# Kernel optimization log

Measured on AMD Instinct MI355X. Metric: run time of the kernel, lower is better.

## Reference

```python
import jax, jax.numpy as jnp
import numpy as np

N_NODES = 10000


def gcn_conv(x, W, b, src, dst, n):
    # GCNConv (PyG defaults): linear transform, add self-loops, symmetric norm,
    # scatter-add aggregation at target nodes, then bias.
    h = x @ W  # [n, out]
    # degree with self-loops: 1 (self) + count of incoming edges per target node
    deg = jnp.ones((n,), h.dtype).at[dst].add(1.0)
    dinv = jax.lax.rsqrt(deg)  # deg >= 1 always
    norm = dinv[src] * dinv[dst]  # [E]
    # edge messages + self-loop contribution (norm_ii = dinv_i^2)
    agg = jnp.zeros_like(h).at[dst].add(h[src] * norm[:, None])
    agg = agg + h * (dinv * dinv)[:, None]
    return agg + b


def setup_inputs() -> dict:
    key = jax.random.key(0)
    ks = jax.random.split(key, 8)
    d_in, d_hid, d_out = 512, 512, 100
    n, e = N_NODES, 160000
    x = jax.random.normal(ks[0], (n, d_in), dtype=jnp.float32)
    edge_index = jax.random.randint(ks[1], (2, e), 0, n, dtype=jnp.int64)
    s1 = 1.0 / np.sqrt(d_in)
    s2 = 1.0 / np.sqrt(d_hid)
    W1 = jax.random.uniform(ks[2], (d_in, d_hid), jnp.float32, -s1, s1)
    b1 = jnp.zeros((d_hid,), jnp.float32)
    W2 = jax.random.uniform(ks[3], (d_hid, d_hid), jnp.float32, -s2, s2)
    b2 = jnp.zeros((d_hid,), jnp.float32)
    Wc = jax.random.uniform(ks[4], (d_hid, d_out), jnp.float32, -s2, s2)
    bc = jax.random.uniform(ks[5], (d_out,), jnp.float32, -s2, s2)
    return {"x": x, "edge_index": edge_index, "W1": W1, "b1": b1,
            "W2": W2, "b2": b2, "Wc": Wc, "bc": bc}


def reference(x, edge_index, W1, b1, W2, b2, Wc, bc):
    src, dst = edge_index[0], edge_index[1]
    n = x.shape[0]
    h = gcn_conv(x, W1, b1, src, dst, n)
    h = jax.nn.relu(h)  # dropout is identity in eval mode
    h = gcn_conv(h, W2, b2, src, dst, n)
    return h @ Wc + bc
```

## Files before the change

kernel.cpp:

```cpp
#include <hip/hip_runtime.h>
#include <hip/hip_bf16.h>
#include <stdint.h>

typedef __bf16 bf16_t;
typedef bf16_t bf16x8 __attribute__((ext_vector_type(8)));
typedef float f32x4 __attribute__((ext_vector_type(4)));

#define NN 10000
#define ELLCAP 64

__device__ __forceinline__ float b2f(unsigned short u) {
  union { unsigned int i; float f; } c; c.i = ((unsigned int)u) << 16; return c.f;
}
__device__ __forceinline__ unsigned short f2b(float f) {
  union { float f; unsigned int i; } c; c.f = f;
  unsigned int x = c.i;
  x += 0x7FFFu + ((x >> 16) & 1u);
  return (unsigned short)(x >> 16);
}
__device__ __forceinline__ uint4 cvt8(float4 a, float4 b) {
  uint4 r;
  r.x = (unsigned int)f2b(a.x) | ((unsigned int)f2b(a.y) << 16);
  r.y = (unsigned int)f2b(a.z) | ((unsigned int)f2b(a.w) << 16);
  r.z = (unsigned int)f2b(b.x) | ((unsigned int)f2b(b.y) << 16);
  r.w = (unsigned int)f2b(b.z) | ((unsigned int)f2b(b.w) << 16);
  return r;
}
__device__ __forceinline__ void load_lds16(const void* g, void* l) {
  __builtin_amdgcn_global_load_lds(
      (const __attribute__((address_space(1))) unsigned int*)g,
      (__attribute__((address_space(3))) unsigned int*)l, 16, 0, 0);
}
__device__ __forceinline__ f32x4 mfma16(bf16x8 a, bf16x8 b, f32x4 c) {
  return __builtin_amdgcn_mfma_f32_16x16x32_bf16(a, b, c, 0, 0, 0);
}

template <bool SCALED>
__device__ void gemm64(const unsigned short* __restrict__ A, const unsigned short* __restrict__ Bt,
                       unsigned short* __restrict__ C, const int* __restrict__ cntp,
                       int M, int Ncols, int ldc, int tm, int tn,
                       unsigned short* __restrict__ As, unsigned short* __restrict__ Bs)
{
  const int tid = threadIdx.x;
  const int lane = tid & 63;
  const int wn = tid >> 6;
  const int quad = lane >> 4, l15 = lane & 15;

  const int r0 = tid >> 2, kc = tid & 3;
  int ga = tm * 64 + r0;  if (ga > M - 1) ga = M - 1;
  const int gb0 = tn * 128 + r0;
  const int gb1 = tn * 128 + 64 + r0;
  const unsigned short* gA  = A + (size_t)ga * 512 + kc * 8;
  const unsigned short* gB0 = Bt + (size_t)gb0 * 512 + kc * 8;
  const unsigned short* gB1 = Bt + (size_t)gb1 * 512 + kc * 8;
  const int loff  = r0 * 32 + kc * 8;
  const int loff1 = (64 + r0) * 32 + kc * 8;
  const int ABUF = 64 * 32, BBUF = 128 * 32;

  f32x4 acc[4][2];
  #pragma unroll
  for (int i = 0; i < 4; i++)
    #pragma unroll
    for (int j = 0; j < 2; j++) {
      f32x4 z = {0.f, 0.f, 0.f, 0.f};
      acc[i][j] = z;
    }

  load_lds16(gA,  &As[loff]);
  load_lds16(gB0, &Bs[loff]);
  load_lds16(gB1, &Bs[loff1]);
  __syncthreads();

  for (int it = 0; it < 16; ++it) {
    const int ca = (it & 1) * ABUF, cb = (it & 1) * BBUF;
    if (it < 15) {
      const int k1 = (it + 1) * 32;
      const int na = ((it & 1) ^ 1) * ABUF, nb = ((it & 1) ^ 1) * BBUF;
      load_lds16(gA + k1,  &As[na + loff]);
      load_lds16(gB0 + k1, &Bs[nb + loff]);
      load_lds16(gB1 + k1, &Bs[nb + loff1]);
    }
    bf16x8 af[4], bfr[2];
    #pragma unroll
    for (int i = 0; i < 4; i++)
      af[i] = *(const bf16x8*)&As[ca + (i * 16 + l15) * 32 + quad * 8];
    #pragma unroll
    for (int j = 0; j < 2; j++)
      bfr[j] = *(const bf16x8*)&Bs[cb + (wn * 32 + j * 16 + l15) * 32 + quad * 8];
    #pragma unroll
    for (int i = 0; i < 4; i++)
      #pragma unroll
      for (int j = 0; j < 2; j++)
        acc[i][j] = mfma16(af[i], bfr[j], acc[i][j]);
    __syncthreads();
  }

  #pragma unroll
  for (int i = 0; i < 4; i++) {
    #pragma unroll
    for (int r = 0; r < 4; r++) {
      const int row = tm * 64 + i * 16 + quad * 4 + r;
      if (row < M) {
        float dv = 1.f;
        if (SCALED) {
          int c = cntp[row]; if (c > ELLCAP) c = ELLCAP;
          dv = rsqrtf((float)(1 + c));
        }
        #pragma unroll
        for (int j = 0; j < 2; j++) {
          const int col = tn * 128 + wn * 32 + j * 16 + l15;
          if (col < Ncols)
            C[(size_t)row * ldc + col] = f2b(acc[i][j][r] * dv);
        }
      }
    }
  }
}

__device__ void wtrans_tile(const float* __restrict__ W, unsigned short* __restrict__ Wt,
                            int ncols, int tr0, int tc0)
{
  __shared__ float tile[64][65];
  const int t = threadIdx.x;
  const int r = t >> 2, c4 = t & 3;
  #pragma unroll
  for (int i = 0; i < 4; i++) {
    int col = c4 * 16 + i * 4;
    int gc = tc0 + col;
    float4 v;
    if (gc + 3 < ncols) {
      v = *(const float4*)&W[(size_t)(tr0 + r) * ncols + gc];
    } else {
      v.x = (gc + 0 < ncols) ? W[(size_t)(tr0 + r) * ncols + gc + 0] : 0.f;
      v.y = (gc + 1 < ncols) ? W[(size_t)(tr0 + r) * ncols + gc + 1] : 0.f;
      v.z = (gc + 2 < ncols) ? W[(size_t)(tr0 + r) * ncols + gc + 2] : 0.f;
      v.w = (gc + 3 < ncols) ? W[(size_t)(tr0 + r) * ncols + gc + 3] : 0.f;
    }
    tile[r][col] = v.x; tile[r][col + 1] = v.y;
    tile[r][col + 2] = v.z; tile[r][col + 3] = v.w;
  }
  __syncthreads();
  const int o = t >> 2;
  #pragma unroll
  for (int i = 0; i < 4; i++) {
    int k = c4 * 16 + i * 4;
    ushort4 u;
    u.x = f2b(tile[k + 0][o]); u.y = f2b(tile[k + 1][o]);
    u.z = f2b(tile[k + 2][o]); u.w = f2b(tile[k + 3][o]);
    *(ushort4*)&Wt[(size_t)(tc0 + o) * 512 + tr0 + k] = u;
  }
}

__global__ __launch_bounds__(256)
void prep_fill(const float* __restrict__ W1, const float* __restrict__ Wc,
               const float* __restrict__ W2, const float* __restrict__ x,
               const int* __restrict__ src, const int* __restrict__ dst,
               int* __restrict__ cnt, int* __restrict__ ell,
               unsigned short* __restrict__ W1t, unsigned short* __restrict__ Wct,
               unsigned short* __restrict__ w2b, unsigned short* __restrict__ xb, int E)
{
  if (blockIdx.x < 64) { wtrans_tile(W1, W1t, 512, (blockIdx.x >> 3) * 64, (blockIdx.x & 7) * 64); return; }
  if (blockIdx.x < 80) { int b = blockIdx.x - 64; wtrans_tile(Wc, Wct, 100, (b >> 1) * 64, (b & 1) * 64); return; }
  const int t0 = (blockIdx.x - 80) * 256 + threadIdx.x;
  const int FT = 256 * 256;
  const float4* W24 = (const float4*)W2;
  uint4* w2b4 = (uint4*)w2b;
  for (int i = t0; i < 512 * 512 / 8; i += FT)
    w2b4[i] = cvt8(W24[i * 2], W24[i * 2 + 1]);
  const float4* x4 = (const float4*)x;
  uint4* xb4 = (uint4*)xb;
  for (int i = t0; i < NN * 512 / 8; i += FT)
    xb4[i] = cvt8(x4[i * 2], x4[i * 2 + 1]);
  for (int e = t0; e < E; e += FT) {
    int s = src[e], d = dst[e];
    int pos = atomicAdd(&cnt[d], 1);
    if (pos < ELLCAP) ell[d * ELLCAP + pos] = s;
  }
}

__global__ __launch_bounds__(256)
void gemm1_fold(const unsigned short* __restrict__ xb, const unsigned short* __restrict__ W1t,
                unsigned short* __restrict__ B2, const int* __restrict__ cnt,
                const unsigned short* __restrict__ Wct, const unsigned short* __restrict__ w2b,
                unsigned short* __restrict__ W2WcT,
                const float* __restrict__ b2, const float* __restrict__ Wc,
                const float* __restrict__ bc, float* __restrict__ bias2c)
{
  __shared__ __align__(16) unsigned short As[2 * 64 * 32];
  __shared__ __align__(16) unsigned short Bs[2 * 128 * 32];
  const int b = blockIdx.x;
  if (b < 628) {
    gemm64<true>(xb, W1t, B2, cnt, NN, 512, 512, b >> 2, b & 3, As, Bs);
  } else if (b < 636) {
    const int g = b - 628;
    gemm64<false>(Wct, w2b, W2WcT, nullptr, 128, 512, 512, g >> 2, g & 3, As, Bs);
  } else {
    const int j = threadIdx.x;
    if (j < 128) {
      float s = 0.f;
      if (j < 100) {
        s = bc[j];
        for (int k = 0; k < 512; k++) s = fmaf(b2[k], Wc[k * 100 + j], s);
      }
      bias2c[j] = s;
    }
  }
}

__device__ __forceinline__ void add8(float* a, uint4 v) {
  a[0] += b2f((unsigned short)(v.x & 0xffffu));
  a[1] += b2f((unsigned short)(v.x >> 16));
  a[2] += b2f((unsigned short)(v.y & 0xffffu));
  a[3] += b2f((unsigned short)(v.y >> 16));
  a[4] += b2f((unsigned short)(v.z & 0xffffu));
  a[5] += b2f((unsigned short)(v.z >> 16));
  a[6] += b2f((unsigned short)(v.w & 0xffffu));
  a[7] += b2f((unsigned short)(v.w >> 16));
}

__global__ __launch_bounds__(256)
void gather1(const unsigned short* __restrict__ h, const int* __restrict__ cnt,
             const int* __restrict__ ell, const float* __restrict__ bias,
             unsigned short* __restrict__ outb, int n)
{
  int node = blockIdx.x * 4 + (threadIdx.x >> 6);
  if (node >= n) return;
  const int lane = threadIdx.x & 63;
  const int c8 = lane * 8;

  int cd = cnt[node]; if (cd > ELLCAP) cd = ELLCAP;
  const float dinv = rsqrtf((float)(1 + cd));
  uint4 hv = *(const uint4*)&h[(size_t)node * 512 + c8];
  float a[8] = {0.f, 0.f, 0.f, 0.f, 0.f, 0.f, 0.f, 0.f};
  add8(a, hv);

  const int* row = ell + node * ELLCAP;
  int j = 0;
  for (; j + 8 <= cd; j += 8) {
    int ss[8]; uint4 vv[8];
    #pragma unroll
    for (int q = 0; q < 8; q++) ss[q] = row[j + q];
    #pragma unroll
    for (int q = 0; q < 8; q++) vv[q] = *(const uint4*)&h[(size_t)ss[q] * 512 + c8];
    #pragma unroll
    for (int q = 0; q < 8; q++) add8(a, vv[q]);
  }
  for (; j < cd; ++j) {
    int s = row[j];
    uint4 v = *(const uint4*)&h[(size_t)s * 512 + c8];
    add8(a, v);
  }

  const float4* bp = (const float4*)&bias[c8];
  float4 b0 = bp[0], b1 = bp[1];
  float bb[8] = {b0.x, b0.y, b0.z, b0.w, b1.x, b1.y, b1.z, b1.w};
  #pragma unroll
  for (int q = 0; q < 8; q++) a[q] = fmaxf(fmaf(a[q], dinv, bb[q]), 0.f);
  uint4 o;
  o.x = (unsigned int)f2b(a[0]) | ((unsigned int)f2b(a[1]) << 16);
  o.y = (unsigned int)f2b(a[2]) | ((unsigned int)f2b(a[3]) << 16);
  o.z = (unsigned int)f2b(a[4]) | ((unsigned int)f2b(a[5]) << 16);
  o.w = (unsigned int)f2b(a[6]) | ((unsigned int)f2b(a[7]) << 16);
  *(uint4*)&outb[(size_t)node * 512 + c8] = o;
}

__global__ __launch_bounds__(256)
void gemm2c(const unsigned short* __restrict__ B1, const unsigned short* __restrict__ W2WcT,
            unsigned short* __restrict__ Z, const int* __restrict__ cnt)
{
  __shared__ __align__(16) unsigned short As[2 * 64 * 32];
  __shared__ __align__(16) unsigned short Bs[2 * 128 * 32];
  gemm64<true>(B1, W2WcT, Z, cnt, NN, 128, 128, blockIdx.x, 0, As, Bs);
}

__global__ __launch_bounds__(256)
void gather2c(const unsigned short* __restrict__ Z, const int* __restrict__ cnt,
              const int* __restrict__ ell, const float* __restrict__ bias2c,
              float* __restrict__ out, int n)
{
  int node = blockIdx.x * 4 + (threadIdx.x >> 6);
  if (node >= n) return;
  const int lane = threadIdx.x & 63;
  const int c2 = lane * 2;

  int cd = cnt[node]; if (cd > ELLCAP) cd = ELLCAP;
  const float dinv = rsqrtf((float)(1 + cd));
  unsigned int hv = *(const unsigned int*)&Z[(size_t)node * 128 + c2];
  float a0 = b2f((unsigned short)(hv & 0xffffu));
  float a1 = b2f((unsigned short)(hv >> 16));

  const int* row = ell + node * ELLCAP;
  int j = 0;
  for (; j + 8 <= cd; j += 8) {
    int ss[8]; unsigned int vv[8];
    #pragma unroll
    for (int q = 0; q < 8; q++) ss[q] = row[j + q];
    #pragma unroll
    for (int q = 0; q < 8; q++) vv[q] = *(const unsigned int*)&Z[(size_t)ss[q] * 128 + c2];
    #pragma unroll
    for (int q = 0; q < 8; q++) {
      a0 += b2f((unsigned short)(vv[q] & 0xffffu));
      a1 += b2f((unsigned short)(vv[q] >> 16));
    }
  }
  for (; j < cd; ++j) {
    int s = row[j];
    unsigned int v = *(const unsigned int*)&Z[(size_t)s * 128 + c2];
    a0 += b2f((unsigned short)(v & 0xffffu));
    a1 += b2f((unsigned short)(v >> 16));
  }
  if (c2 < 100) {
    const float2 bb = *(const float2*)&bias2c[c2];
    *(float2*)&out[(size_t)node * 100 + c2] =
        make_float2(fmaf(a0, dinv, bb.x), fmaf(a1, dinv, bb.y));
  }
}

extern "C" void kernel_launch(void* const* d_in, const int* in_sizes, int n_in,
                              void* d_out, int out_size, void* d_ws, size_t ws_size,
                              hipStream_t stream) {
  const float* x  = (const float*)d_in[0];
  const int*   ei = (const int*)d_in[1];
  const float* W1 = (const float*)d_in[2];
  const float* b1 = (const float*)d_in[3];
  const float* W2 = (const float*)d_in[4];
  const float* b2 = (const float*)d_in[5];
  const float* Wc = (const float*)d_in[6];
  const float* bc = (const float*)d_in[7];
  float* out = (float*)d_out;

  const int n = NN;
  const int E = in_sizes[1] / 2;
  const int* src = ei;
  const int* dst = ei + E;

  char* w = (char*)d_ws;
  int* cnt = (int*)w;                       w += ((n * 4 + 255) / 256) * 256;
  int* ell = (int*)w;                       w += ((n * ELLCAP * 4 + 255) / 256) * 256;
  float* bias2c = (float*)w;                w += 512;
  unsigned short* W1t = (unsigned short*)w; w += 512 * 512 * 2;
  unsigned short* Wct = (unsigned short*)w; w += 128 * 512 * 2;
  unsigned short* w2b = (unsigned short*)w; w += 512 * 512 * 2;
  unsigned short* W2WcT = (unsigned short*)w; w += 128 * 512 * 2;
  unsigned short* B1  = (unsigned short*)w; w += (size_t)n * 512 * 2;
  unsigned short* B2  = (unsigned short*)w; w += (size_t)n * 512 * 2;
  unsigned short* Z   = (unsigned short*)w; w += (size_t)n * 128 * 2;

  unsigned short* xb = B1;

  const int nb_g = (n + 3) / 4;

  hipMemsetAsync(cnt, 0, n * sizeof(int), stream);
  prep_fill<<<336, 256, 0, stream>>>(W1, Wc, W2, x, src, dst, cnt, ell, W1t, Wct, w2b, xb, E);
  gemm1_fold<<<637, 256, 0, stream>>>(xb, W1t, B2, cnt, Wct, w2b, W2WcT, b2, Wc, bc, bias2c);
  gather1<<<nb_g, 256, 0, stream>>>(B2, cnt, ell, b1, B1, n);
  gemm2c<<<157, 256, 0, stream>>>(B1, W2WcT, Z, cnt);
  gather2c<<<nb_g, 256, 0, stream>>>(Z, cnt, ell, bias2c, out, n);
}
```

Measured before the change: 159.1 us.

## Fuse all stages into one persistent kernel with grid barriers

Replaces the five separate kernel launches with a single persistent kernel of 512 blocks. The stages are separated by atomic-counter grid barriers, and each stage loops over its tiles or node blocks. This removes launch overhead and inter-kernel gaps. In exchange, the grid-wide barriers cost something, the spin-wait depends on all 512 blocks being co-resident (with launch_bounds occupancy 2), and fewer blocks run the large GEMM1 phase (637 tiles over 512 blocks).

```diff
diff --git a/kernel.cpp b/kernel.cpp
--- a/kernel.cpp
+++ b/kernel.cpp
@@ -8,6 +8,8 @@
 
 #define NN 10000
 #define ELLCAP 64
+#define GRID 512
+#define NBV 2500
 
 __device__ __forceinline__ float b2f(unsigned short u) {
   union { unsigned int i; float f; } c; c.i = ((unsigned int)u) << 16; return c.f;
@@ -33,6 +35,17 @@
 }
 __device__ __forceinline__ f32x4 mfma16(bf16x8 a, bf16x8 b, f32x4 c) {
   return __builtin_amdgcn_mfma_f32_16x16x32_bf16(a, b, c, 0, 0, 0);
+}
+
+__device__ __forceinline__ void gridbar(int* __restrict__ bar, int idx) {
+  __syncthreads();
+  if (threadIdx.x == 0) {
+    __threadfence();
+    __hip_atomic_fetch_add(&bar[idx], 1, __ATOMIC_ACQ_REL, __HIP_MEMORY_SCOPE_AGENT);
+    while (__hip_atomic_load(&bar[idx], __ATOMIC_ACQUIRE, __HIP_MEMORY_SCOPE_AGENT) < GRID)
+      __builtin_amdgcn_s_sleep(1);
+  }
+  __syncthreads();
 }
 
 template <bool SCALED>
@@ -118,9 +131,8 @@
 }
 
 __device__ void wtrans_tile(const float* __restrict__ W, unsigned short* __restrict__ Wt,
-                            int ncols, int tr0, int tc0)
-{
-  __shared__ float tile[64][65];
+                            int ncols, int tr0, int tc0, float (*tile)[65])
+{
   const int t = threadIdx.x;
   const int r = t >> 2, c4 = t & 3;
   #pragma unroll
@@ -149,20 +161,17 @@
     u.z = f2b(tile[k + 2][o]); u.w = f2b(tile[k + 3][o]);
     *(ushort4*)&Wt[(size_t)(tc0 + o) * 512 + tr0 + k] = u;
   }
-}
-
-__global__ __launch_bounds__(256)
-void prep_fill(const float* __restrict__ W1, const float* __restrict__ Wc,
-               const float* __restrict__ W2, const float* __restrict__ x,
-               const int* __restrict__ src, const int* __restrict__ dst,
-               int* __restrict__ cnt, int* __restrict__ ell,
-               unsigned short* __restrict__ W1t, unsigned short* __restrict__ Wct,
-               unsigned short* __restrict__ w2b, unsigned short* __restrict__ xb, int E)
-{
-  if (blockIdx.x < 64) { wtrans_tile(W1, W1t, 512, (blockIdx.x >> 3) * 64, (blockIdx.x & 7) * 64); return; }
-  if (blockIdx.x < 80) { int b = blockIdx.x - 64; wtrans_tile(Wc, Wct, 100, (b >> 1) * 64, (b & 1) * 64); return; }
-  const int t0 = (blockIdx.x - 80) * 256 + threadIdx.x;
-  const int FT = 256 * 256;
+  __syncthreads();
+}
+
+__device__ void prep_stream(int b, int nstream, const float* __restrict__ W2,
+                            const float* __restrict__ x, const int* __restrict__ src,
+                            const int* __restrict__ dst, int* __restrict__ cnt,
+                            int* __restrict__ ell, unsigned short* __restrict__ w2b,
+                            unsigned short* __restrict__ xb, int E)
+{
+  const int t0 = b * 256 + threadIdx.x;
+  const int FT = nstream * 256;
   const float4* W24 = (const float4*)W2;
   uint4* w2b4 = (uint4*)w2b;
   for (int i = t0; i < 512 * 512 / 8; i += FT)
@@ -178,32 +187,17 @@
   }
 }
 
-__global__ __launch_bounds__(256)
-void gemm1_fold(const unsigned short* __restrict__ xb, const unsigned short* __restrict__ W1t,
-                unsigned short* __restrict__ B2, const int* __restrict__ cnt,
-                const unsigned short* __restrict__ Wct, const unsigned short* __restrict__ w2b,
-                unsigned short* __restrict__ W2WcT,
-                const float* __restrict__ b2, const float* __restrict__ Wc,
-                const float* __restrict__ bc, float* __restrict__ bias2c)
-{
-  __shared__ __align__(16) unsigned short As[2 * 64 * 32];
-  __shared__ __align__(16) unsigned short Bs[2 * 128 * 32];
-  const int b = blockIdx.x;
-  if (b < 628) {
-    gemm64<true>(xb, W1t, B2, cnt, NN, 512, 512, b >> 2, b & 3, As, Bs);
-  } else if (b < 636) {
-    const int g = b - 628;
-    gemm64<false>(Wct, w2b, W2WcT, nullptr, 128, 512, 512, g >> 2, g & 3, As, Bs);
-  } else {
-    const int j = threadIdx.x;
-    if (j < 128) {
-      float s = 0.f;
-      if (j < 100) {
-        s = bc[j];
-        for (int k = 0; k < 512; k++) s = fmaf(b2[k], Wc[k * 100 + j], s);
-      }
-      bias2c[j] = s;
-    }
+__device__ void bias_fold(const float* __restrict__ b2, const float* __restrict__ Wc,
+                          const float* __restrict__ bc, float* __restrict__ bias2c)
+{
+  const int j = threadIdx.x;
+  if (j < 128) {
+    float s = 0.f;
+    if (j < 100) {
+      s = bc[j];
+      for (int k = 0; k < 512; k++) s = fmaf(b2[k], Wc[k * 100 + j], s);
+    }
+    bias2c[j] = s;
   }
 }
 
@@ -218,13 +212,12 @@
   a[7] += b2f((unsigned short)(v.w >> 16));
 }
 
-__global__ __launch_bounds__(256)
-void gather1(const unsigned short* __restrict__ h, const int* __restrict__ cnt,
-             const int* __restrict__ ell, const float* __restrict__ bias,
-             unsigned short* __restrict__ outb, int n)
-{
-  int node = blockIdx.x * 4 + (threadIdx.x >> 6);
-  if (node >= n) return;
+__device__ void gather1_body(int vb, const unsigned short* __restrict__ h,
+                             const int* __restrict__ cnt, const int* __restrict__ ell,
+                             const float* __restrict__ bias, unsigned short* __restrict__ outb)
+{
+  int node = vb * 4 + (threadIdx.x >> 6);
+  if (node >= NN) return;
   const int lane = threadIdx.x & 63;
   const int c8 = lane * 8;
 
@@ -264,22 +257,12 @@
   *(uint4*)&outb[(size_t)node * 512 + c8] = o;
 }
 
-__global__ __launch_bounds__(256)
-void gemm2c(const unsigned short* __restrict__ B1, const unsigned short* __restrict__ W2WcT,
-            unsigned short* __restrict__ Z, const int* __restrict__ cnt)
-{
-  __shared__ __align__(16) unsigned short As[2 * 64 * 32];
-  __shared__ __align__(16) unsigned short Bs[2 * 128 * 32];
-  gemm64<true>(B1, W2WcT, Z, cnt, NN, 128, 128, blockIdx.x, 0, As, Bs);
-}
-
-__global__ __launch_bounds__(256)
-void gather2c(const unsigned short* __restrict__ Z, const int* __restrict__ cnt,
-              const int* __restrict__ ell, const float* __restrict__ bias2c,
-              float* __restrict__ out, int n)
-{
-  int node = blockIdx.x * 4 + (threadIdx.x >> 6);
-  if (node >= n) return;
+__device__ void gather2c_body(int vb, const unsigned short* __restrict__ Z,
+                              const int* __restrict__ cnt, const int* __restrict__ ell,
+                              const float* __restrict__ bias2c, float* __restrict__ out)
+{
+  int node = vb * 4 + (threadIdx.x >> 6);
+  if (node >= NN) return;
   const int lane = threadIdx.x & 63;
   const int c2 = lane * 2;
 
@@ -314,6 +297,44 @@
     *(float2*)&out[(size_t)node * 100 + c2] =
         make_float2(fmaf(a0, dinv, bb.x), fmaf(a1, dinv, bb.y));
   }
+}
+
+__global__ __launch_bounds__(256, 2)
+void fused(const float* __restrict__ x, const int* __restrict__ src, const int* __restrict__ dst,
+           const float* __restrict__ W1, const float* __restrict__ b1,
+           const float* __restrict__ W2, const float* __restrict__ b2,
+           const float* __restrict__ Wc, const float* __restrict__ bc,
+           float* __restrict__ out, int* __restrict__ bar, int* __restrict__ cnt,
+           int* __restrict__ ell, float* __restrict__ bias2c,
+           unsigned short* __restrict__ W1t, unsigned short* __restrict__ Wct,
+           unsigned short* __restrict__ w2b, unsigned short* __restrict__ W2WcT,
+           unsigned short* __restrict__ B1, unsigned short* __restrict__ B2,
+           unsigned short* __restrict__ Z, unsigned short* __restrict__ xb, int E)
+{
+  __shared__ __align__(16) unsigned char smem[24576];
+  unsigned short* As = (unsigned short*)smem;
+  unsigned short* Bs = (unsigned short*)(smem + 8192);
+  const int b = blockIdx.x;
+
+  if (b < 64)      wtrans_tile(W1, W1t, 512, (b >> 3) * 64, (b & 7) * 64, (float(*)[65])smem);
+  else if (b < 80) { int t = b - 64; wtrans_tile(Wc, Wct, 100, (t >> 1) * 64, (t & 1) * 64, (float(*)[65])smem); }
+  else             prep_stream(b - 80, GRID - 80, W2, x, src, dst, cnt, ell, w2b, xb, E);
+  gridbar(bar, 0);
+
+  for (int t = b; t < 637; t += GRID) {
+    if (t < 628)      gemm64<true>(xb, W1t, B2, cnt, NN, 512, 512, t >> 2, t & 3, As, Bs);
+    else if (t < 636) { int g = t - 628; gemm64<false>(Wct, w2b, W2WcT, nullptr, 128, 512, 512, g >> 2, g & 3, As, Bs); }
+    else              bias_fold(b2, Wc, bc, bias2c);
+  }
+  gridbar(bar, 1);
+
+  for (int vb = b; vb < NBV; vb += GRID) gather1_body(vb, B2, cnt, ell, b1, B1);
+  gridbar(bar, 2);
+
+  if (b < 157) gemm64<true>(B1, W2WcT, Z, cnt, NN, 128, 128, b, 0, As, Bs);
+  gridbar(bar, 3);
+
+  for (int vb = b; vb < NBV; vb += GRID) gather2c_body(vb, Z, cnt, ell, bias2c, out);
 }
 
 extern "C" void kernel_launch(void* const* d_in, const int* in_sizes, int n_in,
@@ -330,11 +351,12 @@
   float* out = (float*)d_out;
 
   const int n = NN;
-  const int E = in_sizes[1] / 2;
+  int E = in_sizes[1] / 2;
   const int* src = ei;
   const int* dst = ei + E;
 
   char* w = (char*)d_ws;
+  int* bar = (int*)w;                       w += 256;
   int* cnt = (int*)w;                       w += ((n * 4 + 255) / 256) * 256;
   int* ell = (int*)w;                       w += ((n * ELLCAP * 4 + 255) / 256) * 256;
   float* bias2c = (float*)w;                w += 512;
@@ -348,12 +370,12 @@
 
   unsigned short* xb = B1;
 
-  const int nb_g = (n + 3) / 4;
-
-  hipMemsetAsync(cnt, 0, n * sizeof(int), stream);
-  prep_fill<<<336, 256, 0, stream>>>(W1, Wc, W2, x, src, dst, cnt, ell, W1t, Wct, w2b, xb, E);
-  gemm1_fold<<<637, 256, 0, stream>>>(xb, W1t, B2, cnt, Wct, w2b, W2WcT, b2, Wc, bc, bias2c);
-  gather1<<<nb_g, 256, 0, stream>>>(B2, cnt, ell, b1, B1, n);
-  gemm2c<<<157, 256, 0, stream>>>(B1, W2WcT, Z, cnt);
-  gather2c<<<nb_g, 256, 0, stream>>>(Z, cnt, ell, bias2c, out, n);
-}
+  hipMemsetAsync(bar, 0, 256 + ((n * 4 + 255) / 256) * 256, stream);
+
+  void* args[] = {(void*)&x, (void*)&src, (void*)&dst, (void*)&W1, (void*)&b1,
+                  (void*)&W2, (void*)&b2, (void*)&Wc, (void*)&bc, (void*)&out,
+                  (void*)&bar, (void*)&cnt, (void*)&ell, (void*)&bias2c,
+                  (void*)&W1t, (void*)&Wct, (void*)&w2b, (void*)&W2WcT,
+                  (void*)&B1, (void*)&B2, (void*)&Z, (void*)&xb, (void*)&E};
+  hipLaunchKernel((const void*)fused, dim3(GRID), dim3(256), args, 0, stream);
+}
```

Result: slower. 612.8 us (+285.1%).

## Fuse fp32-to-bf16 conversion of x into first GEMM load path

Applied to the files above, without the earlier changes.

The separate pass that converts x from fp32 to bf16 in the prep kernel is dropped. The first GEMM now reads fp32 x directly and converts it in registers while staging to LDS, with the global load for the next K-step issued before the MFMAs of the current one. This removes a full write and reread of the 10000x512 bf16 copy. It also remaps block indices so that contiguous tile ranges go to each XCD, aiming for better L2 locality, and it shrinks the prep grid. In exchange the GEMM reads twice as many A bytes, and the conversion adds register pressure inside the main loop.

```diff
diff --git a/kernel.cpp b/kernel.cpp
--- a/kernel.cpp
+++ b/kernel.cpp
@@ -117,6 +117,88 @@
   }
 }
 
+__device__ void gemm64_f32A(const float* __restrict__ A, const unsigned short* __restrict__ Bt,
+                            unsigned short* __restrict__ C, const int* __restrict__ cntp,
+                            int M, int tm, int tn,
+                            unsigned short* __restrict__ As, unsigned short* __restrict__ Bs)
+{
+  const int tid = threadIdx.x;
+  const int lane = tid & 63;
+  const int wn = tid >> 6;
+  const int quad = lane >> 4, l15 = lane & 15;
+
+  const int r0 = tid >> 2, kc = tid & 3;
+  int ga = tm * 64 + r0;  if (ga > M - 1) ga = M - 1;
+  const int gb0 = tn * 128 + r0;
+  const int gb1 = tn * 128 + 64 + r0;
+  const float* gA = A + (size_t)ga * 512 + kc * 8;
+  const unsigned short* gB0 = Bt + (size_t)gb0 * 512 + kc * 8;
+  const unsigned short* gB1 = Bt + (size_t)gb1 * 512 + kc * 8;
+  const int loff  = r0 * 32 + kc * 8;
+  const int loff1 = (64 + r0) * 32 + kc * 8;
+  const int ABUF = 64 * 32, BBUF = 128 * 32;
+
+  f32x4 acc[4][2];
+  #pragma unroll
+  for (int i = 0; i < 4; i++)
+    #pragma unroll
+    for (int j = 0; j < 2; j++) {
+      f32x4 z = {0.f, 0.f, 0.f, 0.f};
+      acc[i][j] = z;
+    }
+
+  {
+    float4 a0 = *(const float4*)(gA), a1 = *(const float4*)(gA + 4);
+    *(uint4*)&As[loff] = cvt8(a0, a1);
+    load_lds16(gB0, &Bs[loff]);
+    load_lds16(gB1, &Bs[loff1]);
+  }
+  __syncthreads();
+
+  for (int it = 0; it < 16; ++it) {
+    const int ca = (it & 1) * ABUF, cb = (it & 1) * BBUF;
+    const int na = ((it & 1) ^ 1) * ABUF, nb = ((it & 1) ^ 1) * BBUF;
+    float4 a0, a1;
+    if (it < 15) {
+      const int k1 = (it + 1) * 32;
+      a0 = *(const float4*)(gA + k1);  a1 = *(const float4*)(gA + k1 + 4);
+      load_lds16(gB0 + k1, &Bs[nb + loff]);
+      load_lds16(gB1 + k1, &Bs[nb + loff1]);
+    }
+    bf16x8 af[4], bfr[2];
+    #pragma unroll
+    for (int i = 0; i < 4; i++)
+      af[i] = *(const bf16x8*)&As[ca + (i * 16 + l15) * 32 + quad * 8];
+    #pragma unroll
+    for (int j = 0; j < 2; j++)
+      bfr[j] = *(const bf16x8*)&Bs[cb + (wn * 32 + j * 16 + l15) * 32 + quad * 8];
+    #pragma unroll
+    for (int i = 0; i < 4; i++)
+      #pragma unroll
+      for (int j = 0; j < 2; j++)
+        acc[i][j] = mfma16(af[i], bfr[j], acc[i][j]);
+    if (it < 15) *(uint4*)&As[na + loff] = cvt8(a0, a1);
+    __syncthreads();
+  }
+
+  #pragma unroll
+  for (int i = 0; i < 4; i++) {
+    #pragma unroll
+    for (int r = 0; r < 4; r++) {
+      const int row = tm * 64 + i * 16 + quad * 4 + r;
+      if (row < M) {
+        int c = cntp[row]; if (c > ELLCAP) c = ELLCAP;
+        const float dv = rsqrtf((float)(1 + c));
+        #pragma unroll
+        for (int j = 0; j < 2; j++) {
+          const int col = tn * 128 + wn * 32 + j * 16 + l15;
+          C[(size_t)row * 512 + col] = f2b(acc[i][j][r] * dv);
+        }
+      }
+    }
+  }
+}
+
 __device__ void wtrans_tile(const float* __restrict__ W, unsigned short* __restrict__ Wt,
                             int ncols, int tr0, int tc0)
 {
@@ -153,24 +235,19 @@
 
 __global__ __launch_bounds__(256)
 void prep_fill(const float* __restrict__ W1, const float* __restrict__ Wc,
-               const float* __restrict__ W2, const float* __restrict__ x,
-               const int* __restrict__ src, const int* __restrict__ dst,
-               int* __restrict__ cnt, int* __restrict__ ell,
-               unsigned short* __restrict__ W1t, unsigned short* __restrict__ Wct,
-               unsigned short* __restrict__ w2b, unsigned short* __restrict__ xb, int E)
+               const float* __restrict__ W2, const int* __restrict__ src,
+               const int* __restrict__ dst, int* __restrict__ cnt,
+               int* __restrict__ ell, unsigned short* __restrict__ W1t,
+               unsigned short* __restrict__ Wct, unsigned short* __restrict__ w2b, int E)
 {
   if (blockIdx.x < 64) { wtrans_tile(W1, W1t, 512, (blockIdx.x >> 3) * 64, (blockIdx.x & 7) * 64); return; }
   if (blockIdx.x < 80) { int b = blockIdx.x - 64; wtrans_tile(Wc, Wct, 100, (b >> 1) * 64, (b & 1) * 64); return; }
   const int t0 = (blockIdx.x - 80) * 256 + threadIdx.x;
-  const int FT = 256 * 256;
+  const int FT = 160 * 256;
   const float4* W24 = (const float4*)W2;
   uint4* w2b4 = (uint4*)w2b;
   for (int i = t0; i < 512 * 512 / 8; i += FT)
     w2b4[i] = cvt8(W24[i * 2], W24[i * 2 + 1]);
-  const float4* x4 = (const float4*)x;
-  uint4* xb4 = (uint4*)xb;
-  for (int i = t0; i < NN * 512 / 8; i += FT)
-    xb4[i] = cvt8(x4[i * 2], x4[i * 2 + 1]);
   for (int e = t0; e < E; e += FT) {
     int s = src[e], d = dst[e];
     int pos = atomicAdd(&cnt[d], 1);
@@ -179,7 +256,7 @@
 }
 
 __global__ __launch_bounds__(256)
-void gemm1_fold(const unsigned short* __restrict__ xb, const unsigned short* __restrict__ W1t,
+void gemm1_fold(const float* __restrict__ x, const unsigned short* __restrict__ W1t,
                 unsigned short* __restrict__ B2, const int* __restrict__ cnt,
                 const unsigned short* __restrict__ Wct, const unsigned short* __restrict__ w2b,
                 unsigned short* __restrict__ W2WcT,
@@ -190,7 +267,10 @@
   __shared__ __align__(16) unsigned short Bs[2 * 128 * 32];
   const int b = blockIdx.x;
   if (b < 628) {
-    gemm64<true>(xb, W1t, B2, cnt, NN, 512, 512, b >> 2, b & 3, As, Bs);
+    const int xcd = b & 7, loc = b >> 3;
+    const int base = (xcd < 4) ? xcd * 79 : 316 + (xcd - 4) * 78;
+    const int t = base + loc;
+    gemm64_f32A(x, W1t, B2, cnt, NN, t >> 2, t & 3, As, Bs);
   } else if (b < 636) {
     const int g = b - 628;
     gemm64<false>(Wct, w2b, W2WcT, nullptr, 128, 512, 512, g >> 2, g & 3, As, Bs);
@@ -346,13 +426,11 @@
   unsigned short* B2  = (unsigned short*)w; w += (size_t)n * 512 * 2;
   unsigned short* Z   = (unsigned short*)w; w += (size_t)n * 128 * 2;
 
-  unsigned short* xb = B1;
-
   const int nb_g = (n + 3) / 4;
 
   hipMemsetAsync(cnt, 0, n * sizeof(int), stream);
-  prep_fill<<<336, 256, 0, stream>>>(W1, Wc, W2, x, src, dst, cnt, ell, W1t, Wct, w2b, xb, E);
-  gemm1_fold<<<637, 256, 0, stream>>>(xb, W1t, B2, cnt, Wct, w2b, W2WcT, b2, Wc, bc, bias2c);
+  prep_fill<<<240, 256, 0, stream>>>(W1, Wc, W2, src, dst, cnt, ell, W1t, Wct, w2b, E);
+  gemm1_fold<<<637, 256, 0, stream>>>(x, W1t, B2, cnt, Wct, w2b, W2WcT, b2, Wc, bc, bias2c);
   gather1<<<nb_g, 256, 0, stream>>>(B2, cnt, ell, b1, B1, n);
   gemm2c<<<157, 256, 0, stream>>>(B1, W2WcT, Z, cnt);
   gather2c<<<nb_g, 256, 0, stream>>>(Z, cnt, ell, bias2c, out, n);
```

Measured after the change: 156.9 us. Within noise of the previous version (-1.4%).
